# Optimization experiments

Hardware: AMD Instinct MI355X
Metric: run time of the kernel (lower is better)

The kernel has to match this reference:

```python
import jax, jax.numpy as jnp
import numpy as np

N = 50000      # nodes
E = 800000     # edges (before self-loops)
H = 4          # heads
NEG_SLOPE = 0.2
EPS = 1e-16


def setup_inputs() -> dict:
    key = jax.random.key(0)
    ks = jax.random.split(key, 10)
    m, hidden, m_y = 128, 32, 32
    x = jax.random.normal(ks[0], (N, m), jnp.float32)
    edge_index = jax.random.randint(ks[1], (2, E), 0, N, jnp.int32)
    s1 = 1.0 / np.sqrt(m)
    s2 = 1.0 / np.sqrt(H * hidden)
    W1 = jax.random.normal(ks[2], (m, H * hidden), jnp.float32) * s1
    a1_src = jax.random.normal(ks[3], (H, hidden), jnp.float32) * s1
    a1_dst = jax.random.normal(ks[4], (H, hidden), jnp.float32) * s1
    b1 = jnp.zeros((H * hidden,), jnp.float32)
    W2 = jax.random.normal(ks[5], (H * hidden, H * m_y), jnp.float32) * s2
    a2_src = jax.random.normal(ks[6], (H, m_y), jnp.float32) * s2
    a2_dst = jax.random.normal(ks[7], (H, m_y), jnp.float32) * s2
    b2 = jnp.zeros((H * m_y,), jnp.float32)
    return {"x": x, "edge_index": edge_index, "W1": W1, "a1_src": a1_src,
            "a1_dst": a1_dst, "b1": b1, "W2": W2, "a2_src": a2_src,
            "a2_dst": a2_dst, "b2": b2}


def gat_conv(x, W, a_src, a_dst, bias, src, dst):
    # x: [N, F_in], W: [F_in, H*C]
    C = a_src.shape[1]
    h = (x @ W).reshape(N, H, C)                      # [N, H, C]
    alpha_s = jnp.einsum('nhc,hc->nh', h, a_src)       # [N, H]
    alpha_d = jnp.einsum('nhc,hc->nh', h, a_dst)       # [N, H]
    e = jax.nn.leaky_relu(alpha_s[src] + alpha_d[dst], NEG_SLOPE)  # [Etot, H]
    # segment softmax over incoming edges of each dst node
    e_max = jax.ops.segment_max(e, dst, num_segments=N)            # [N, H]
    e_exp = jnp.exp(e - e_max[dst])
    denom = jax.ops.segment_sum(e_exp, dst, num_segments=N)        # [N, H]
    alpha = e_exp / (denom[dst] + EPS)                             # [Etot, H]
    out = jax.ops.segment_sum(h[src] * alpha[:, :, None], dst, num_segments=N)
    return out.reshape(N, H * C) + bias


def reference(x, edge_index, W1, a1_src, a1_dst, b1, W2, a2_src, a2_dst, b2):
    # add self-loops (PyG GATConv default add_self_loops=True)
    loops = jnp.arange(N, dtype=edge_index.dtype)
    src = jnp.concatenate([edge_index[0], loops])
    dst = jnp.concatenate([edge_index[1], loops])
    out = gat_conv(x, W1, a1_src, a1_dst, b1, src, dst)
    out = jax.nn.elu(out)
    # dropout(p=0.8) is identity in eval mode
    out = gat_conv(out, W2, a2_src, a2_dst, b2, src, dst)
    return out
```

## Files before the change

### kernel.cpp

```cpp
#include <hip/hip_runtime.h>
#include <math.h>
#include <stdint.h>

static __device__ __forceinline__ float lrelu(float x) { return x >= 0.f ? x : 0.2f * x; }

static __device__ __forceinline__ uint32_t f2bf(float f) {
    uint32_t u = __float_as_uint(f);
    return (u + 0x7FFFu + ((u >> 16) & 1u)) >> 16;
}

__global__ __launch_bounds__(256) void count_rank(const int* __restrict__ dst, int E,
                                                  int* __restrict__ deg,
                                                  int* __restrict__ rank) {
    int i = blockIdx.x * 256 + threadIdx.x;
    if (i < E) rank[i] = atomicAdd(&deg[dst[i]], 1);
}

__global__ __launch_bounds__(256) void scan1(const int* __restrict__ deg, int N, int ntot,
                                             int* __restrict__ rowptr, int* __restrict__ csum) {
    __shared__ int s[256];
    int t = threadIdx.x;
    int i = blockIdx.x * 256 + t;
    int v = (i < N) ? deg[i] : 0;
    s[t] = v;
    __syncthreads();
    #pragma unroll
    for (int off = 1; off < 256; off <<= 1) {
        int add = (t >= off) ? s[t - off] : 0;
        __syncthreads();
        s[t] += add;
        __syncthreads();
    }
    if (i < ntot) rowptr[i] = s[t] - v;
    if (t == 255) csum[blockIdx.x] = s[255];
}

__global__ __launch_bounds__(256) void scan2(const int* __restrict__ csum,
                                             int* __restrict__ coff, int nch) {
    __shared__ int s[256];
    int t = threadIdx.x;
    int v = (t < nch) ? csum[t] : 0;
    s[t] = v;
    __syncthreads();
    #pragma unroll
    for (int off = 1; off < 256; off <<= 1) {
        int add = (t >= off) ? s[t - off] : 0;
        __syncthreads();
        s[t] += add;
        __syncthreads();
    }
    coff[t] = s[t] - v;
}

__global__ __launch_bounds__(256) void scan3(int* __restrict__ rowptr,
                                             const int* __restrict__ coff, int ntot) {
    int i = blockIdx.x * 256 + threadIdx.x;
    if (i < ntot) rowptr[i] += coff[blockIdx.x];
}

__global__ __launch_bounds__(256) void fill_csr(const int* __restrict__ src,
                                                const int* __restrict__ dst,
                                                const int* __restrict__ rank, int E,
                                                const int* __restrict__ rowptr,
                                                int* __restrict__ colidx) {
    int i = blockIdx.x * 256 + threadIdx.x;
    if (i < E) colidx[rowptr[dst[i]] + rank[i]] = src[i];
}

__global__ __launch_bounds__(256) void gemm_alpha(const float* __restrict__ x,
                                                  const float* __restrict__ W,
                                                  const float* __restrict__ a_src,
                                                  const float* __restrict__ a_dst,
                                                  uint32_t* __restrict__ hbf,
                                                  float* __restrict__ as_,
                                                  float* __restrict__ ad_,
                                                  int nrows) {
    __shared__ float xs[128 * 32];
    __shared__ float ws[32 * 128];
    const int t = threadIdx.x;
    const int row0 = blockIdx.x * 128;
    const int rg = t >> 4;
    const int cg = t & 15;
    const int r0 = rg * 8;
    const int c0 = cg * 8;

    float acc[8][8];
    #pragma unroll
    for (int j = 0; j < 8; ++j)
        #pragma unroll
        for (int c = 0; c < 8; ++c) acc[j][c] = 0.f;

    const float4* x4 = (const float4*)x;
    const float4* W4 = (const float4*)W;
    float4* xs4 = (float4*)xs;
    float4* ws4 = (float4*)ws;

    for (int kc = 0; kc < 4; ++kc) {
        #pragma unroll
        for (int i = 0; i < 4; ++i) {
            int idx = t + i * 256;
            int r = idx >> 3, q = idx & 7;
            float4 v = make_float4(0.f, 0.f, 0.f, 0.f);
            if (row0 + r < nrows) v = x4[(size_t)(row0 + r) * 32 + kc * 8 + q];
            xs4[idx] = v;
        }
        #pragma unroll
        for (int i = 0; i < 4; ++i) {
            int idx = t + i * 256;
            ws4[idx] = W4[kc * 1024 + idx];
        }
        __syncthreads();

        #pragma unroll 2
        for (int kk = 0; kk < 32; kk += 4) {
            float4 xv[8];
            #pragma unroll
            for (int j = 0; j < 8; ++j)
                xv[j] = xs4[(r0 + j) * 8 + (kk >> 2)];
            #pragma unroll
            for (int k2 = 0; k2 < 4; ++k2) {
                int k = kk + k2;
                float4 wv0 = ws4[k * 32 + cg * 2];
                float4 wv1 = ws4[k * 32 + cg * 2 + 1];
                #pragma unroll
                for (int j = 0; j < 8; ++j) {
                    float xk = (k2 == 0) ? xv[j].x : (k2 == 1) ? xv[j].y
                             : (k2 == 2) ? xv[j].z : xv[j].w;
                    acc[j][0] = fmaf(xk, wv0.x, acc[j][0]);
                    acc[j][1] = fmaf(xk, wv0.y, acc[j][1]);
                    acc[j][2] = fmaf(xk, wv0.z, acc[j][2]);
                    acc[j][3] = fmaf(xk, wv0.w, acc[j][3]);
                    acc[j][4] = fmaf(xk, wv1.x, acc[j][4]);
                    acc[j][5] = fmaf(xk, wv1.y, acc[j][5]);
                    acc[j][6] = fmaf(xk, wv1.z, acc[j][6]);
                    acc[j][7] = fmaf(xk, wv1.w, acc[j][7]);
                }
            }
        }
        __syncthreads();
    }

    const int hd = cg >> 2;
    float asv[8], adv[8];
    #pragma unroll
    for (int cc = 0; cc < 8; ++cc) {
        asv[cc] = a_src[c0 + cc];
        adv[cc] = a_dst[c0 + cc];
    }
    #pragma unroll
    for (int j = 0; j < 8; ++j) {
        int r = row0 + r0 + j;
        float ps = 0.f, pd = 0.f;
        #pragma unroll
        for (int cc = 0; cc < 8; ++cc) {
            ps = fmaf(acc[j][cc], asv[cc], ps);
            pd = fmaf(acc[j][cc], adv[cc], pd);
        }
        ps += __shfl_xor(ps, 1); ps += __shfl_xor(ps, 2);
        pd += __shfl_xor(pd, 1); pd += __shfl_xor(pd, 2);
        if (r < nrows) {
            uint4 pk;
            pk.x = f2bf(acc[j][0]) | (f2bf(acc[j][1]) << 16);
            pk.y = f2bf(acc[j][2]) | (f2bf(acc[j][3]) << 16);
            pk.z = f2bf(acc[j][4]) | (f2bf(acc[j][5]) << 16);
            pk.w = f2bf(acc[j][6]) | (f2bf(acc[j][7]) << 16);
            *(uint4*)&hbf[(size_t)r * 64 + cg * 4] = pk;
            if ((cg & 3) == 0) {
                as_[r * 4 + hd] = ps;
                ad_[r * 4 + hd] = pd;
            }
        }
    }
}

__global__ __launch_bounds__(256) void aggregate(const uint32_t* __restrict__ hb,
                                                 const float* __restrict__ as_,
                                                 const float* __restrict__ ad_,
                                                 const int* __restrict__ rowptr,
                                                 const int* __restrict__ colidx,
                                                 const float* __restrict__ bias,
                                                 float* __restrict__ out, int n, int do_elu) {
    int node = blockIdx.x * 4 + (threadIdx.x >> 6);
    if (node >= n) return;
    int lane = threadIdx.x & 63;
    int hd = lane >> 4;
    int k = lane * 2;
    int c = lane & 31;
    int ce = c >> 2;
    int ch = c & 3;
    float adn = ad_[node * 4 + hd];
    float adc = ad_[node * 4 + ch];
    float accx = 0.f, accy = 0.f, denom = 0.f;

    {
        float wgt = __expf(lrelu(as_[node * 4 + hd] + adn));
        uint32_t u = hb[(size_t)node * 64 + lane];
        accx = fmaf(wgt, __uint_as_float(u << 16), accx);
        accy = fmaf(wgt, __uint_as_float(u & 0xFFFF0000u), accy);
        denom += wgt;
    }
    const int beg = rowptr[node], end = rowptr[node + 1];
    int j = beg;
    for (; j + 8 <= end; j += 8) {
        int s0 = colidx[j],     s1 = colidx[j + 1];
        int s2 = colidx[j + 2], s3 = colidx[j + 3];
        int s4 = colidx[j + 4], s5 = colidx[j + 5];
        int s6 = colidx[j + 6], s7 = colidx[j + 7];
        int sw = colidx[j + ce];
        float aw = as_[sw * 4 + ch];
        uint32_t u0 = hb[(size_t)s0 * 64 + lane], u1 = hb[(size_t)s1 * 64 + lane];
        uint32_t u2 = hb[(size_t)s2 * 64 + lane], u3 = hb[(size_t)s3 * 64 + lane];
        uint32_t u4 = hb[(size_t)s4 * 64 + lane], u5 = hb[(size_t)s5 * 64 + lane];
        uint32_t u6 = hb[(size_t)s6 * 64 + lane], u7 = hb[(size_t)s7 * 64 + lane];
        float w = __expf(lrelu(aw + adc));
        float w0 = __shfl(w, 0  + hd), w1 = __shfl(w, 4  + hd);
        float w2 = __shfl(w, 8  + hd), w3 = __shfl(w, 12 + hd);
        float w4 = __shfl(w, 16 + hd), w5 = __shfl(w, 20 + hd);
        float w6 = __shfl(w, 24 + hd), w7 = __shfl(w, 28 + hd);
        accx = fmaf(w0, __uint_as_float(u0 << 16), accx);
        accy = fmaf(w0, __uint_as_float(u0 & 0xFFFF0000u), accy);
        accx = fmaf(w1, __uint_as_float(u1 << 16), accx);
        accy = fmaf(w1, __uint_as_float(u1 & 0xFFFF0000u), accy);
        accx = fmaf(w2, __uint_as_float(u2 << 16), accx);
        accy = fmaf(w2, __uint_as_float(u2 & 0xFFFF0000u), accy);
        accx = fmaf(w3, __uint_as_float(u3 << 16), accx);
        accy = fmaf(w3, __uint_as_float(u3 & 0xFFFF0000u), accy);
        accx = fmaf(w4, __uint_as_float(u4 << 16), accx);
        accy = fmaf(w4, __uint_as_float(u4 & 0xFFFF0000u), accy);
        accx = fmaf(w5, __uint_as_float(u5 << 16), accx);
        accy = fmaf(w5, __uint_as_float(u5 & 0xFFFF0000u), accy);
        accx = fmaf(w6, __uint_as_float(u6 << 16), accx);
        accy = fmaf(w6, __uint_as_float(u6 & 0xFFFF0000u), accy);
        accx = fmaf(w7, __uint_as_float(u7 << 16), accx);
        accy = fmaf(w7, __uint_as_float(u7 & 0xFFFF0000u), accy);
        denom += ((w0 + w1) + (w2 + w3)) + ((w4 + w5) + (w6 + w7));
    }
    for (; j < end; ++j) {
        int src = colidx[j];
        float wgt = __expf(lrelu(as_[src * 4 + hd] + adn));
        uint32_t u = hb[(size_t)src * 64 + lane];
        accx = fmaf(wgt, __uint_as_float(u << 16), accx);
        accy = fmaf(wgt, __uint_as_float(u & 0xFFFF0000u), accy);
        denom += wgt;
    }
    float inv = 1.f / (denom + 1e-16f);
    float o0 = fmaf(accx, inv, bias[k]);
    float o1 = fmaf(accy, inv, bias[k + 1]);
    if (do_elu) {
        o0 = o0 > 0.f ? o0 : (__expf(o0) - 1.f);
        o1 = o1 > 0.f ? o1 : (__expf(o1) - 1.f);
    }
    *(float2*)&out[(size_t)node * 128 + k] = make_float2(o0, o1);
}

extern "C" void kernel_launch(void* const* d_in, const int* in_sizes, int n_in,
                              void* d_out, int out_size, void* d_ws, size_t ws_size,
                              hipStream_t stream) {
    const float* x   = (const float*)d_in[0];
    const int*   ei  = (const int*)d_in[1];
    const float* W1  = (const float*)d_in[2];
    const float* a1s = (const float*)d_in[3];
    const float* a1d = (const float*)d_in[4];
    const float* b1  = (const float*)d_in[5];
    const float* W2  = (const float*)d_in[6];
    const float* a2s = (const float*)d_in[7];
    const float* a2d = (const float*)d_in[8];
    const float* b2  = (const float*)d_in[9];
    float* out = (float*)d_out;

    const int N = in_sizes[0] / 128;
    const int E = in_sizes[1] / 2;
    const int* esrc = ei;
    const int* edst = ei + E;

    char* w = (char*)d_ws;
    uint32_t* hbf  = (uint32_t*)w; w += (size_t)N * 64 * 4;
    float*    as_  = (float*)w;    w += (size_t)N * 4 * 4;
    float*    ad_  = (float*)w;    w += (size_t)N * 4 * 4;
    int* deg    = (int*)w;   w += (size_t)N * 4;
    int* rowptr = (int*)w;   w += (size_t)(N + 1) * 4;
    int* rank   = (int*)w;   w += (size_t)E * 4;
    int* colidx = (int*)w;   w += (size_t)E * 4;
    int* csum   = (int*)w;   w += 256 * 4;
    int* coff   = (int*)w;   w += 256 * 4;
    float* out1 = out;

    hipMemsetAsync(deg, 0, (size_t)N * 4, stream);

    const int eb = (E + 255) / 256;
    const int ntot = N + 1;
    const int nch = (ntot + 255) / 256;

    count_rank<<<eb, 256, 0, stream>>>(edst, E, deg, rank);
    scan1<<<nch, 256, 0, stream>>>(deg, N, ntot, rowptr, csum);
    scan2<<<1, 256, 0, stream>>>(csum, coff, nch);
    scan3<<<nch, 256, 0, stream>>>(rowptr, coff, ntot);
    fill_csr<<<eb, 256, 0, stream>>>(esrc, edst, rank, E, rowptr, colidx);

    const int gb = (N + 127) / 128;
    const int nb = (N + 3) / 4;

    gemm_alpha<<<gb, 256, 0, stream>>>(x, W1, a1s, a1d, hbf, as_, ad_, N);
    aggregate<<<nb, 256, 0, stream>>>(hbf, as_, ad_, rowptr, colidx, b1, out1, N, 1);

    gemm_alpha<<<gb, 256, 0, stream>>>(out1, W2, a2s, a2d, hbf, as_, ad_, N);
    aggregate<<<nb, 256, 0, stream>>>(hbf, as_, ad_, rowptr, colidx, b2, out, N, 0);
}
```

Measured before the change: 300.1 us.

## Pad CSR rows to multiples of eight and fuse first GEMM with degree counting

Each destination row in the CSR is padded to a multiple of 8 with a dummy source node N. That node's attention logit is set to -1e30, so its weight becomes zero and the scalar tail loop in aggregate can be removed. The first GEMM+alpha kernel and the atomic degree-count kernel now run as one launch, with blocks split by index, so they overlap and one launch is saved. The cost is extra padded edges, an extra pad-fill kernel, and a larger workspace. The hbf row for the dummy node is never written, so uninitialized data times a zero weight could produce NaN.

```diff
diff --git a/kernel.cpp b/kernel.cpp
--- a/kernel.cpp
+++ b/kernel.cpp
@@ -9,76 +9,17 @@
     return (u + 0x7FFFu + ((u >> 16) & 1u)) >> 16;
 }
 
-__global__ __launch_bounds__(256) void count_rank(const int* __restrict__ dst, int E,
-                                                  int* __restrict__ deg,
-                                                  int* __restrict__ rank) {
-    int i = blockIdx.x * 256 + threadIdx.x;
-    if (i < E) rank[i] = atomicAdd(&deg[dst[i]], 1);
-}
-
-__global__ __launch_bounds__(256) void scan1(const int* __restrict__ deg, int N, int ntot,
-                                             int* __restrict__ rowptr, int* __restrict__ csum) {
-    __shared__ int s[256];
-    int t = threadIdx.x;
-    int i = blockIdx.x * 256 + t;
-    int v = (i < N) ? deg[i] : 0;
-    s[t] = v;
-    __syncthreads();
-    #pragma unroll
-    for (int off = 1; off < 256; off <<= 1) {
-        int add = (t >= off) ? s[t - off] : 0;
-        __syncthreads();
-        s[t] += add;
-        __syncthreads();
-    }
-    if (i < ntot) rowptr[i] = s[t] - v;
-    if (t == 255) csum[blockIdx.x] = s[255];
-}
-
-__global__ __launch_bounds__(256) void scan2(const int* __restrict__ csum,
-                                             int* __restrict__ coff, int nch) {
-    __shared__ int s[256];
-    int t = threadIdx.x;
-    int v = (t < nch) ? csum[t] : 0;
-    s[t] = v;
-    __syncthreads();
-    #pragma unroll
-    for (int off = 1; off < 256; off <<= 1) {
-        int add = (t >= off) ? s[t - off] : 0;
-        __syncthreads();
-        s[t] += add;
-        __syncthreads();
-    }
-    coff[t] = s[t] - v;
-}
-
-__global__ __launch_bounds__(256) void scan3(int* __restrict__ rowptr,
-                                             const int* __restrict__ coff, int ntot) {
-    int i = blockIdx.x * 256 + threadIdx.x;
-    if (i < ntot) rowptr[i] += coff[blockIdx.x];
-}
-
-__global__ __launch_bounds__(256) void fill_csr(const int* __restrict__ src,
-                                                const int* __restrict__ dst,
-                                                const int* __restrict__ rank, int E,
-                                                const int* __restrict__ rowptr,
-                                                int* __restrict__ colidx) {
-    int i = blockIdx.x * 256 + threadIdx.x;
-    if (i < E) colidx[rowptr[dst[i]] + rank[i]] = src[i];
-}
-
-__global__ __launch_bounds__(256) void gemm_alpha(const float* __restrict__ x,
-                                                  const float* __restrict__ W,
-                                                  const float* __restrict__ a_src,
-                                                  const float* __restrict__ a_dst,
-                                                  uint32_t* __restrict__ hbf,
-                                                  float* __restrict__ as_,
-                                                  float* __restrict__ ad_,
-                                                  int nrows) {
-    __shared__ float xs[128 * 32];
-    __shared__ float ws[32 * 128];
+static __device__ void gemm_alpha_body(const float* __restrict__ x,
+                                       const float* __restrict__ W,
+                                       const float* __restrict__ a_src,
+                                       const float* __restrict__ a_dst,
+                                       uint32_t* __restrict__ hbf,
+                                       float* __restrict__ as_,
+                                       float* __restrict__ ad_,
+                                       int nrows, int blk,
+                                       float* xs, float* ws) {
     const int t = threadIdx.x;
-    const int row0 = blockIdx.x * 128;
+    const int row0 = blk * 128;
     const int rg = t >> 4;
     const int cg = t & 15;
     const int r0 = rg * 8;
@@ -173,6 +114,107 @@
     }
 }
 
+__global__ __launch_bounds__(256) void gemm_count(const float* __restrict__ x,
+                                                  const float* __restrict__ W,
+                                                  const float* __restrict__ a_src,
+                                                  const float* __restrict__ a_dst,
+                                                  uint32_t* __restrict__ hbf,
+                                                  float* __restrict__ as_,
+                                                  float* __restrict__ ad_,
+                                                  int nrows, int gb,
+                                                  const int* __restrict__ dst, int E,
+                                                  int* __restrict__ deg,
+                                                  int* __restrict__ rank) {
+    __shared__ float xs[128 * 32];
+    __shared__ float ws[32 * 128];
+    if ((int)blockIdx.x < gb) {
+        gemm_alpha_body(x, W, a_src, a_dst, hbf, as_, ad_, nrows, blockIdx.x, xs, ws);
+    } else {
+        int i = (blockIdx.x - gb) * 256 + threadIdx.x;
+        if (i < E) rank[i] = atomicAdd(&deg[dst[i]], 1);
+    }
+}
+
+__global__ __launch_bounds__(256) void gemm_alpha(const float* __restrict__ x,
+                                                  const float* __restrict__ W,
+                                                  const float* __restrict__ a_src,
+                                                  const float* __restrict__ a_dst,
+                                                  uint32_t* __restrict__ hbf,
+                                                  float* __restrict__ as_,
+                                                  float* __restrict__ ad_,
+                                                  int nrows) {
+    __shared__ float xs[128 * 32];
+    __shared__ float ws[32 * 128];
+    gemm_alpha_body(x, W, a_src, a_dst, hbf, as_, ad_, nrows, blockIdx.x, xs, ws);
+}
+
+__global__ __launch_bounds__(256) void scan1(const int* __restrict__ deg, int N, int ntot,
+                                             int* __restrict__ rowptr, int* __restrict__ csum) {
+    __shared__ int s[256];
+    int t = threadIdx.x;
+    int i = blockIdx.x * 256 + t;
+    int v = (i < N) ? ((deg[i] + 7) & ~7) : 0;
+    s[t] = v;
+    __syncthreads();
+    #pragma unroll
+    for (int off = 1; off < 256; off <<= 1) {
+        int add = (t >= off) ? s[t - off] : 0;
+        __syncthreads();
+        s[t] += add;
+        __syncthreads();
+    }
+    if (i < ntot) rowptr[i] = s[t] - v;
+    if (t == 255) csum[blockIdx.x] = s[255];
+}
+
+__global__ __launch_bounds__(256) void scan2(const int* __restrict__ csum,
+                                             int* __restrict__ coff, int nch) {
+    __shared__ int s[256];
+    int t = threadIdx.x;
+    int v = (t < nch) ? csum[t] : 0;
+    s[t] = v;
+    __syncthreads();
+    #pragma unroll
+    for (int off = 1; off < 256; off <<= 1) {
+        int add = (t >= off) ? s[t - off] : 0;
+        __syncthreads();
+        s[t] += add;
+        __syncthreads();
+    }
+    coff[t] = s[t] - v;
+}
+
+__global__ __launch_bounds__(256) void scan3(int* __restrict__ rowptr,
+                                             const int* __restrict__ coff, int ntot) {
+    int i = blockIdx.x * 256 + threadIdx.x;
+    if (i < ntot) rowptr[i] += coff[blockIdx.x];
+}
+
+__global__ __launch_bounds__(256) void pad_fill(const int* __restrict__ deg,
+                                                const int* __restrict__ rowptr,
+                                                int* __restrict__ colidx,
+                                                float* __restrict__ as_, int N) {
+    int i = blockIdx.x * 256 + threadIdx.x;
+    if (i == 0) {
+        as_[N * 4 + 0] = -1e30f; as_[N * 4 + 1] = -1e30f;
+        as_[N * 4 + 2] = -1e30f; as_[N * 4 + 3] = -1e30f;
+    }
+    if (i < N) {
+        int b = rowptr[i] + deg[i];
+        int e = rowptr[i + 1];
+        for (int p = b; p < e; ++p) colidx[p] = N;
+    }
+}
+
+__global__ __launch_bounds__(256) void fill_csr(const int* __restrict__ src,
+                                                const int* __restrict__ dst,
+                                                const int* __restrict__ rank, int E,
+                                                const int* __restrict__ rowptr,
+                                                int* __restrict__ colidx) {
+    int i = blockIdx.x * 256 + threadIdx.x;
+    if (i < E) colidx[rowptr[dst[i]] + rank[i]] = src[i];
+}
+
 __global__ __launch_bounds__(256) void aggregate(const uint32_t* __restrict__ hb,
                                                  const float* __restrict__ as_,
                                                  const float* __restrict__ ad_,
@@ -200,8 +242,7 @@
         denom += wgt;
     }
     const int beg = rowptr[node], end = rowptr[node + 1];
-    int j = beg;
-    for (; j + 8 <= end; j += 8) {
+    for (int j = beg; j < end; j += 8) {
         int s0 = colidx[j],     s1 = colidx[j + 1];
         int s2 = colidx[j + 2], s3 = colidx[j + 3];
         int s4 = colidx[j + 4], s5 = colidx[j + 5];
@@ -235,14 +276,6 @@
         accy = fmaf(w7, __uint_as_float(u7 & 0xFFFF0000u), accy);
         denom += ((w0 + w1) + (w2 + w3)) + ((w4 + w5) + (w6 + w7));
     }
-    for (; j < end; ++j) {
-        int src = colidx[j];
-        float wgt = __expf(lrelu(as_[src * 4 + hd] + adn));
-        uint32_t u = hb[(size_t)src * 64 + lane];
-        accx = fmaf(wgt, __uint_as_float(u << 16), accx);
-        accy = fmaf(wgt, __uint_as_float(u & 0xFFFF0000u), accy);
-        denom += wgt;
-    }
     float inv = 1.f / (denom + 1e-16f);
     float o0 = fmaf(accx, inv, bias[k]);
     float o1 = fmaf(accy, inv, bias[k + 1]);
@@ -274,13 +307,13 @@
     const int* edst = ei + E;
 
     char* w = (char*)d_ws;
-    uint32_t* hbf  = (uint32_t*)w; w += (size_t)N * 64 * 4;
-    float*    as_  = (float*)w;    w += (size_t)N * 4 * 4;
-    float*    ad_  = (float*)w;    w += (size_t)N * 4 * 4;
+    uint32_t* hbf  = (uint32_t*)w; w += (size_t)(N + 1) * 64 * 4;
+    float*    as_  = (float*)w;    w += (size_t)(N + 1) * 4 * 4;
+    float*    ad_  = (float*)w;    w += (size_t)(N + 1) * 4 * 4;
     int* deg    = (int*)w;   w += (size_t)N * 4;
     int* rowptr = (int*)w;   w += (size_t)(N + 1) * 4;
     int* rank   = (int*)w;   w += (size_t)E * 4;
-    int* colidx = (int*)w;   w += (size_t)E * 4;
+    int* colidx = (int*)w;   w += ((size_t)E + 8ull * N) * 4;
     int* csum   = (int*)w;   w += 256 * 4;
     int* coff   = (int*)w;   w += 256 * 4;
     float* out1 = out;
@@ -290,17 +323,18 @@
     const int eb = (E + 255) / 256;
     const int ntot = N + 1;
     const int nch = (ntot + 255) / 256;
-
-    count_rank<<<eb, 256, 0, stream>>>(edst, E, deg, rank);
+    const int gb = (N + 127) / 128;
+    const int nb = (N + 3) / 4;
+    const int pb = (N + 255) / 256;
+
+    gemm_count<<<gb + eb, 256, 0, stream>>>(x, W1, a1s, a1d, hbf, as_, ad_, N, gb,
+                                            edst, E, deg, rank);
     scan1<<<nch, 256, 0, stream>>>(deg, N, ntot, rowptr, csum);
     scan2<<<1, 256, 0, stream>>>(csum, coff, nch);
     scan3<<<nch, 256, 0, stream>>>(rowptr, coff, ntot);
+    pad_fill<<<pb, 256, 0, stream>>>(deg, rowptr, colidx, as_, N);
     fill_csr<<<eb, 256, 0, stream>>>(esrc, edst, rank, E, rowptr, colidx);
 
-    const int gb = (N + 127) / 128;
-    const int nb = (N + 3) / 4;
-
-    gemm_alpha<<<gb, 256, 0, stream>>>(x, W1, a1s, a1d, hbf, as_, ad_, N);
     aggregate<<<nb, 256, 0, stream>>>(hbf, as_, ad_, rowptr, colidx, b1, out1, N, 1);
 
     gemm_alpha<<<gb, 256, 0, stream>>>(out1, W2, a2s, a2d, hbf, as_, ad_, N);
```

Result: slower. 334.7 us (+11.5%).

## Pad CSR rows to multiples of 16 with dummy node and drop tail loop

Applied to the files above, without the earlier changes.

Each node's CSR row is rounded up to a multiple of 16. The padding slots point to a dummy node N whose attention logit is -1e30 and whose features are zero, so they add nothing. The aggregate kernel then handles 16 edges per iteration with no scalar remainder loop, which removes divergent tail work and gives more memory-level parallelism. The cost is extra padded edge traffic (on average about 7.5 per node, against roughly 16 real edges per node) plus a pad-fill kernel. The GEMM's shared-memory W layout is also permuted so the two float4 loads per k sit in separate halves, which may reduce LDS bank conflicts.

```diff
diff --git a/kernel.cpp b/kernel.cpp
--- a/kernel.cpp
+++ b/kernel.cpp
@@ -21,7 +21,7 @@
     __shared__ int s[256];
     int t = threadIdx.x;
     int i = blockIdx.x * 256 + t;
-    int v = (i < N) ? deg[i] : 0;
+    int v = (i < N) ? ((deg[i] + 15) & ~15) : 0;
     s[t] = v;
     __syncthreads();
     #pragma unroll
@@ -56,6 +56,21 @@
                                              const int* __restrict__ coff, int ntot) {
     int i = blockIdx.x * 256 + threadIdx.x;
     if (i < ntot) rowptr[i] += coff[blockIdx.x];
+}
+
+__global__ __launch_bounds__(256) void pad_fill(const int* __restrict__ deg,
+                                                const int* __restrict__ rowptr,
+                                                int* __restrict__ colidx,
+                                                float* __restrict__ as_,
+                                                uint32_t* __restrict__ hbf, int N) {
+    int i = blockIdx.x * 256 + threadIdx.x;
+    if (i < 4) as_[N * 4 + i] = -1e30f;
+    if (i < 64) hbf[(size_t)N * 64 + i] = 0u;
+    if (i < N) {
+        int b = rowptr[i] + deg[i];
+        int e = rowptr[i + 1];
+        for (int p = b; p < e; ++p) colidx[p] = N;
+    }
 }
 
 __global__ __launch_bounds__(256) void fill_csr(const int* __restrict__ src,
@@ -107,7 +122,9 @@
         #pragma unroll
         for (int i = 0; i < 4; ++i) {
             int idx = t + i * 256;
-            ws4[idx] = W4[kc * 1024 + idx];
+            int kk2 = idx >> 5, q = idx & 31;
+            int dq = (q & 1) ? (16 + (q >> 1)) : (q >> 1);
+            ws4[kk2 * 32 + dq] = W4[kc * 1024 + idx];
         }
         __syncthreads();
 
@@ -120,8 +137,8 @@
             #pragma unroll
             for (int k2 = 0; k2 < 4; ++k2) {
                 int k = kk + k2;
-                float4 wv0 = ws4[k * 32 + cg * 2];
-                float4 wv1 = ws4[k * 32 + cg * 2 + 1];
+                float4 wv0 = ws4[k * 32 + cg];
+                float4 wv1 = ws4[k * 32 + 16 + cg];
                 #pragma unroll
                 for (int j = 0; j < 8; ++j) {
                     float xk = (k2 == 0) ? xv[j].x : (k2 == 1) ? xv[j].y
@@ -185,9 +202,8 @@
     int lane = threadIdx.x & 63;
     int hd = lane >> 4;
     int k = lane * 2;
-    int c = lane & 31;
-    int ce = c >> 2;
-    int ch = c & 3;
+    int ce = lane >> 2;
+    int ch = lane & 3;
     float adn = ad_[node * 4 + hd];
     float adc = ad_[node * 4 + ch];
     float accx = 0.f, accy = 0.f, denom = 0.f;
@@ -200,48 +216,23 @@
         denom += wgt;
     }
     const int beg = rowptr[node], end = rowptr[node + 1];
-    int j = beg;
-    for (; j + 8 <= end; j += 8) {
-        int s0 = colidx[j],     s1 = colidx[j + 1];
-        int s2 = colidx[j + 2], s3 = colidx[j + 3];
-        int s4 = colidx[j + 4], s5 = colidx[j + 5];
-        int s6 = colidx[j + 6], s7 = colidx[j + 7];
+    for (int j = beg; j < end; j += 16) {
+        int sE[16];
+        #pragma unroll
+        for (int e = 0; e < 16; ++e) sE[e] = colidx[j + e];
         int sw = colidx[j + ce];
         float aw = as_[sw * 4 + ch];
-        uint32_t u0 = hb[(size_t)s0 * 64 + lane], u1 = hb[(size_t)s1 * 64 + lane];
-        uint32_t u2 = hb[(size_t)s2 * 64 + lane], u3 = hb[(size_t)s3 * 64 + lane];
-        uint32_t u4 = hb[(size_t)s4 * 64 + lane], u5 = hb[(size_t)s5 * 64 + lane];
-        uint32_t u6 = hb[(size_t)s6 * 64 + lane], u7 = hb[(size_t)s7 * 64 + lane];
+        uint32_t u[16];
+        #pragma unroll
+        for (int e = 0; e < 16; ++e) u[e] = hb[(size_t)sE[e] * 64 + lane];
         float w = __expf(lrelu(aw + adc));
-        float w0 = __shfl(w, 0  + hd), w1 = __shfl(w, 4  + hd);
-        float w2 = __shfl(w, 8  + hd), w3 = __shfl(w, 12 + hd);
-        float w4 = __shfl(w, 16 + hd), w5 = __shfl(w, 20 + hd);
-        float w6 = __shfl(w, 24 + hd), w7 = __shfl(w, 28 + hd);
-        accx = fmaf(w0, __uint_as_float(u0 << 16), accx);
-        accy = fmaf(w0, __uint_as_float(u0 & 0xFFFF0000u), accy);
-        accx = fmaf(w1, __uint_as_float(u1 << 16), accx);
-        accy = fmaf(w1, __uint_as_float(u1 & 0xFFFF0000u), accy);
-        accx = fmaf(w2, __uint_as_float(u2 << 16), accx);
-        accy = fmaf(w2, __uint_as_float(u2 & 0xFFFF0000u), accy);
-        accx = fmaf(w3, __uint_as_float(u3 << 16), accx);
-        accy = fmaf(w3, __uint_as_float(u3 & 0xFFFF0000u), accy);
-        accx = fmaf(w4, __uint_as_float(u4 << 16), accx);
-        accy = fmaf(w4, __uint_as_float(u4 & 0xFFFF0000u), accy);
-        accx = fmaf(w5, __uint_as_float(u5 << 16), accx);
-        accy = fmaf(w5, __uint_as_float(u5 & 0xFFFF0000u), accy);
-        accx = fmaf(w6, __uint_as_float(u6 << 16), accx);
-        accy = fmaf(w6, __uint_as_float(u6 & 0xFFFF0000u), accy);
-        accx = fmaf(w7, __uint_as_float(u7 << 16), accx);
-        accy = fmaf(w7, __uint_as_float(u7 & 0xFFFF0000u), accy);
-        denom += ((w0 + w1) + (w2 + w3)) + ((w4 + w5) + (w6 + w7));
-    }
-    for (; j < end; ++j) {
-        int src = colidx[j];
-        float wgt = __expf(lrelu(as_[src * 4 + hd] + adn));
-        uint32_t u = hb[(size_t)src * 64 + lane];
-        accx = fmaf(wgt, __uint_as_float(u << 16), accx);
-        accy = fmaf(wgt, __uint_as_float(u & 0xFFFF0000u), accy);
-        denom += wgt;
+        #pragma unroll
+        for (int e = 0; e < 16; ++e) {
+            float we = __shfl(w, e * 4 + hd);
+            accx = fmaf(we, __uint_as_float(u[e] << 16), accx);
+            accy = fmaf(we, __uint_as_float(u[e] & 0xFFFF0000u), accy);
+            denom += we;
+        }
     }
     float inv = 1.f / (denom + 1e-16f);
     float o0 = fmaf(accx, inv, bias[k]);
@@ -274,13 +265,13 @@
     const int* edst = ei + E;
 
     char* w = (char*)d_ws;
-    uint32_t* hbf  = (uint32_t*)w; w += (size_t)N * 64 * 4;
-    float*    as_  = (float*)w;    w += (size_t)N * 4 * 4;
-    float*    ad_  = (float*)w;    w += (size_t)N * 4 * 4;
+    uint32_t* hbf  = (uint32_t*)w; w += (size_t)(N + 1) * 64 * 4;
+    float*    as_  = (float*)w;    w += (size_t)(N + 1) * 4 * 4;
+    float*    ad_  = (float*)w;    w += (size_t)(N + 1) * 4 * 4;
     int* deg    = (int*)w;   w += (size_t)N * 4;
     int* rowptr = (int*)w;   w += (size_t)(N + 1) * 4;
     int* rank   = (int*)w;   w += (size_t)E * 4;
-    int* colidx = (int*)w;   w += (size_t)E * 4;
+    int* colidx = (int*)w;   w += ((size_t)E + 16ull * N) * 4;
     int* csum   = (int*)w;   w += 256 * 4;
     int* coff   = (int*)w;   w += 256 * 4;
     float* out1 = out;
@@ -290,15 +281,16 @@
     const int eb = (E + 255) / 256;
     const int ntot = N + 1;
     const int nch = (ntot + 255) / 256;
+    const int gb = (N + 127) / 128;
+    const int nb = (N + 3) / 4;
+    const int pb = (N + 255) / 256;
 
     count_rank<<<eb, 256, 0, stream>>>(edst, E, deg, rank);
     scan1<<<nch, 256, 0, stream>>>(deg, N, ntot, rowptr, csum);
     scan2<<<1, 256, 0, stream>>>(csum, coff, nch);
     scan3<<<nch, 256, 0, stream>>>(rowptr, coff, ntot);
+    pad_fill<<<pb, 256, 0, stream>>>(deg, rowptr, colidx, as_, hbf, N);
     fill_csr<<<eb, 256, 0, stream>>>(esrc, edst, rank, E, rowptr, colidx);
-
-    const int gb = (N + 127) / 128;
-    const int nb = (N + 3) / 4;
 
     gemm_alpha<<<gb, 256, 0, stream>>>(x, W1, a1s, a1d, hbf, as_, ad_, N);
     aggregate<<<nb, 256, 0, stream>>>(hbf, as_, ad_, rowptr, colidx, b1, out1, N, 1);
```

After: 294.1 us. 1.02x faster.
